# Performance work log

Hardware: AMD Instinct MI355X
Metric: run time of the kernel (lower is better)

## Reference

```python
import jax, jax.numpy as jnp
import numpy as np

S, H, E, DFF = 8192, 1024, 8, 4096
CAPACITY = (S * 1) // E  # capacity_factor=1.0, k=1 -> 1024 (>= min_capacity 4)


def setup_inputs() -> dict:
    key = jax.random.key(0)
    ks = jax.random.split(key, 6)
    sc_in = 1.0 / np.sqrt(H)
    sc_ff = 1.0 / np.sqrt(DFF)
    return {
        "hidden_states": jax.random.normal(ks[0], (S, H), dtype=jnp.float32),
        "wg": jax.random.normal(ks[1], (H, E), dtype=jnp.float32) * sc_in,
        "w1": jax.random.normal(ks[2], (E, H, DFF), dtype=jnp.float32) * sc_in,
        "b1": jnp.zeros((E, DFF), dtype=jnp.float32),
        "w2": jax.random.normal(ks[3], (E, DFF, H), dtype=jnp.float32) * sc_ff,
        "b2": jnp.zeros((E, H), dtype=jnp.float32),
    }


def _top1_gate(x, wg):
    # DeepSpeed top1gating (noisy_gate_policy=None, used_token=None)
    logits = x @ wg                                   # [S, E]
    gates = jax.nn.softmax(logits, axis=-1)           # [S, E]
    idx = jnp.argmax(gates, axis=-1)                  # [S]
    mask1 = jax.nn.one_hot(idx, E, dtype=gates.dtype) # [S, E]
    # load-balancing aux loss (uses pre-capacity mask)
    me = jnp.mean(gates, axis=0)
    ce = jnp.mean(mask1, axis=0)
    l_aux = jnp.sum(me * ce) * E
    # capacity-based token dropping
    locations1 = jnp.cumsum(mask1, axis=0) - 1.0      # position within expert
    mask1 = mask1 * (locations1 < CAPACITY)
    exp_counts = jnp.sum(mask1, axis=0).astype(jnp.int32)
    loc_s = jnp.sum(locations1 * mask1, axis=1).astype(jnp.int32)   # [S]
    loc_sc = jax.nn.one_hot(loc_s, CAPACITY, dtype=gates.dtype)     # [S, C]
    combine = jnp.einsum("se,sc->sec", gates * mask1, loc_sc)       # [S, E, C]
    dispatch = (combine > 0).astype(gates.dtype)
    return l_aux, combine, dispatch, exp_counts


def reference(hidden_states, wg, w1, b1, w2, b2):
    l_aux, combine, dispatch, exp_counts = _top1_gate(hidden_states, wg)
    # dispatch tokens to expert slots: [E, C, H]
    disp = jnp.einsum("sec,sh->ech", dispatch, hidden_states)
    # grouped expert FFN (GELU MLP)
    h1 = jax.nn.gelu(jnp.einsum("ech,ehf->ecf", disp, w1) + b1[:, None, :])
    eo = jnp.einsum("ecf,efh->ech", h1, w2) + b2[:, None, :]
    # combine back to token order, weighted by gate values
    out = jnp.einsum("sec,ech->sh", combine, eo)      # [S, H]
    # dropout prob = 0.0 -> identity
    return out, l_aux, exp_counts
```

## Files before the change

kernel.cpp:

```cpp
#include <hip/hip_runtime.h>

#define S_TOK 8192
#define H_DIM 1024
#define NE    8
#define CAP   1024
#define DFF   4096

typedef unsigned short u16;
typedef __bf16 bf16_t;
typedef bf16_t bf16x8 __attribute__((ext_vector_type(8)));
typedef float  f32x4  __attribute__((ext_vector_type(4)));

__device__ __forceinline__ u16 f2bf(float f) {
  union { float f; unsigned u; } a; a.f = f;
  unsigned u = a.u;
  u += 0x7fffu + ((u >> 16) & 1u);
  return (u16)(u >> 16);
}

__device__ __forceinline__ float gelu_tanh(float x) {
  const float c = 0.7978845608028654f;
  float t = tanhf(c * (x + 0.044715f * x * x * x));
  return 0.5f * x * (1.0f + t);
}

__global__ void gate_kernel(const float* __restrict__ x, const float* __restrict__ wg,
                            float* __restrict__ gate, int* __restrict__ expert,
                            int* __restrict__ rank, int* __restrict__ blockCnt,
                            float* __restrict__ blockMe) {
  __shared__ float sg[16][8];
  __shared__ int   se[16];
  int tid = threadIdx.x, lane = tid & 63, w = tid >> 6;
  int b = blockIdx.x;
  for (int j = 0; j < 4; ++j) {
    int t = w * 4 + j;
    int s = b * 16 + t;
    const float* xr = x + (size_t)s * H_DIM;
    float acc[8];
#pragma unroll
    for (int e = 0; e < 8; ++e) acc[e] = 0.f;
#pragma unroll
    for (int i = 0; i < 16; ++i) {
      int h = i * 64 + lane;
      float xv = xr[h];
      float4 wa = *(const float4*)(wg + h * 8);
      float4 wb = *(const float4*)(wg + h * 8 + 4);
      acc[0] += xv * wa.x; acc[1] += xv * wa.y; acc[2] += xv * wa.z; acc[3] += xv * wa.w;
      acc[4] += xv * wb.x; acc[5] += xv * wb.y; acc[6] += xv * wb.z; acc[7] += xv * wb.w;
    }
#pragma unroll
    for (int off = 32; off >= 1; off >>= 1)
#pragma unroll
      for (int e = 0; e < 8; ++e) acc[e] += __shfl_down(acc[e], off);
    if (lane == 0) {
      float mx = acc[0];
#pragma unroll
      for (int e = 1; e < 8; ++e) mx = fmaxf(mx, acc[e]);
      float g[8], Z = 0.f;
#pragma unroll
      for (int e = 0; e < 8; ++e) { g[e] = expf(acc[e] - mx); Z += g[e]; }
      int am = 0; float best = acc[0];
#pragma unroll
      for (int e = 1; e < 8; ++e) if (acc[e] > best) { best = acc[e]; am = e; }
      float inv = 1.f / Z;
#pragma unroll
      for (int e = 0; e < 8; ++e) sg[t][e] = g[e] * inv;
      se[t] = am;
      gate[s] = g[am] * inv;
      expert[s] = am;
    }
  }
  __syncthreads();
  if (tid < 16) {
    int e = se[tid], r = 0;
    for (int t2 = 0; t2 < tid; ++t2) r += (se[t2] == e) ? 1 : 0;
    rank[b * 16 + tid] = r;
  }
  if (tid < 8) {
    int c = 0; float m = 0.f;
#pragma unroll
    for (int t = 0; t < 16; ++t) { c += (se[t] == tid) ? 1 : 0; m += sg[t][tid]; }
    blockCnt[b * 8 + tid] = c;
    blockMe[b * 8 + tid] = m;
  }
}

__global__ void scan_kernel(const int* __restrict__ blockCnt, const float* __restrict__ blockMe,
                            int* __restrict__ blockOff, int* __restrict__ counts,
                            float* __restrict__ tail) {
  int tid = threadIdx.x;
  int e = tid >> 6, lane = tid & 63;
  int run = 0; float msum = 0.f;
  for (int c = 0; c < 8; ++c) {
    int b = c * 64 + lane;
    int v = blockCnt[b * 8 + e];
    float mv = blockMe[b * 8 + e];
    int sc = v;
#pragma unroll
    for (int off = 1; off < 64; off <<= 1) {
      int u = __shfl_up(sc, off);
      if (lane >= off) sc += u;
    }
    blockOff[b * 8 + e] = run + sc - v;
    run += __shfl(sc, 63);
#pragma unroll
    for (int off = 32; off >= 1; off >>= 1) mv += __shfl_down(mv, off);
    msum += __shfl(mv, 0);
  }
  __shared__ float sm[8];
  __shared__ int scnt[8];
  if (lane == 0) {
    sm[e] = msum; scnt[e] = run;
    counts[e] = run < CAP ? run : CAP;
  }
  __syncthreads();
  if (tid == 0) {
    float la = 0.f;
    for (int i = 0; i < 8; ++i)
      la += (sm[i] / (float)S_TOK) * ((float)scnt[i] / (float)S_TOK);
    tail[0] = la * (float)NE;
    for (int i = 0; i < 8; ++i) {
      int cc = scnt[i] < CAP ? scnt[i] : CAP;
      tail[1 + i] = (float)cc;
    }
  }
}

__global__ void assign_kernel(const int* __restrict__ expert, const int* __restrict__ rank,
                              const int* __restrict__ blockOff, int* __restrict__ slot_token) {
  int s = blockIdx.x * 256 + threadIdx.x;
  int e = expert[s];
  int pos = blockOff[(s >> 4) * 8 + e] + rank[s];
  if (pos < CAP) slot_token[e * CAP + pos] = s;
}

__global__ void gather_kernel(const float* __restrict__ x, const int* __restrict__ slot_token,
                              const int* __restrict__ counts, u16* __restrict__ disp) {
  int slot = blockIdx.x;
  int e = slot >> 10, c = slot & 1023;
  int t = threadIdx.x;
  ushort4 v4;
  if (c < counts[e]) {
    int s = slot_token[slot];
    float4 v = *(const float4*)(x + (size_t)s * H_DIM + t * 4);
    v4.x = f2bf(v.x); v4.y = f2bf(v.y); v4.z = f2bf(v.z); v4.w = f2bf(v.w);
  } else {
    v4.x = 0; v4.y = 0; v4.z = 0; v4.w = 0;
  }
  *(ushort4*)(disp + (size_t)slot * H_DIM + t * 4) = v4;
}

__global__ void transpose_convert(const float* __restrict__ src0, u16* __restrict__ dst0,
                                  int R, int C) {
  __shared__ float tile[64][65];
  int e = blockIdx.z;
  const float* src = src0 + (size_t)e * R * C;
  u16* dst = dst0 + (size_t)e * R * C;
  int c0 = blockIdx.x * 64, r0 = blockIdx.y * 64;
  int g = threadIdx.x & 15, rr = threadIdx.x >> 4;
#pragma unroll
  for (int p = 0; p < 4; ++p) {
    int r = rr + p * 16;
    float4 v = *(const float4*)(src + (size_t)(r0 + r) * C + c0 + g * 4);
    tile[r][g * 4 + 0] = v.x;
    tile[r][g * 4 + 1] = v.y;
    tile[r][g * 4 + 2] = v.z;
    tile[r][g * 4 + 3] = v.w;
  }
  __syncthreads();
#pragma unroll
  for (int p = 0; p < 4; ++p) {
    int c = rr + p * 16;
    ushort4 o;
    o.x = f2bf(tile[g * 4 + 0][c]);
    o.y = f2bf(tile[g * 4 + 1][c]);
    o.z = f2bf(tile[g * 4 + 2][c]);
    o.w = f2bf(tile[g * 4 + 3][c]);
    *(ushort4*)(dst + (size_t)(c0 + c) * R + r0 + g * 4) = o;
  }
}

__device__ __forceinline__ void stage_tile(const u16* g, int ldk, u16* lds) {
  int tid = threadIdx.x;
  int lane = tid & 63, w = tid >> 6;
#pragma unroll
  for (int r = 0; r < 2; ++r) {
    int p = (w * 2 + r) * 64 + lane;
    int row = p >> 2;
    int kq = (p & 3) ^ ((row >> 1) & 3);
    const u16* gp = g + (size_t)row * ldk + kq * 8;
    u16* lp = lds + (w * 2 + r) * 512;
    __builtin_amdgcn_global_load_lds((__attribute__((address_space(1))) int*)(gp),
                                     (__attribute__((address_space(3))) int*)(lp),
                                     16, 0, 0);
  }
}

template <int KDIM>
__device__ __forceinline__ void gemm_core(const u16* A, const u16* Bt, int lda, int ldb,
                                          u16* As, u16* Bs, f32x4 acc[4][4]) {
  int tid = threadIdx.x;
  int lane = tid & 63;
  int w = tid >> 6, wm = w >> 1, wn = w & 1;
  int q = lane >> 4, l15 = lane & 15;
  int aoff[4], boff[4];
#pragma unroll
  for (int t = 0; t < 4; ++t) {
    int ra = wm * 64 + t * 16 + l15;
    aoff[t] = ra * 32 + ((q ^ ((ra >> 1) & 3)) * 8);
    int rb = wn * 64 + t * 16 + l15;
    boff[t] = rb * 32 + ((q ^ ((rb >> 1) & 3)) * 8);
  }
  for (int kt = 0; kt < KDIM; kt += 32) {
    stage_tile(A + kt, lda, As);
    stage_tile(Bt + kt, ldb, Bs);
    __syncthreads();
    bf16x8 af[4], bfr[4];
#pragma unroll
    for (int t = 0; t < 4; ++t) af[t] = *(const bf16x8*)(As + aoff[t]);
#pragma unroll
    for (int t = 0; t < 4; ++t) bfr[t] = *(const bf16x8*)(Bs + boff[t]);
#pragma unroll
    for (int mt = 0; mt < 4; ++mt)
#pragma unroll
      for (int nt = 0; nt < 4; ++nt)
        acc[mt][nt] = __builtin_amdgcn_mfma_f32_16x16x32_bf16(af[mt], bfr[nt], acc[mt][nt], 0, 0, 0);
    __syncthreads();
  }
}

__global__ __launch_bounds__(256, 2) void gemm1_kernel(const u16* __restrict__ disp,
                                                       const u16* __restrict__ w1t,
                                                       const float* __restrict__ b1,
                                                       u16* __restrict__ h1) {
  __shared__ __align__(16) u16 As[4096];
  __shared__ __align__(16) u16 Bs[4096];
  int e = blockIdx.z;
  int m0 = blockIdx.y * 128, n0 = blockIdx.x * 128;
  const u16* A  = disp + (size_t)e * CAP * H_DIM + (size_t)m0 * H_DIM;
  const u16* Bt = w1t + (size_t)e * DFF * H_DIM + (size_t)n0 * H_DIM;
  f32x4 acc[4][4];
  f32x4 zero = {0.f, 0.f, 0.f, 0.f};
#pragma unroll
  for (int i = 0; i < 4; ++i)
#pragma unroll
    for (int j = 0; j < 4; ++j) acc[i][j] = zero;
  gemm_core<H_DIM>(A, Bt, H_DIM, H_DIM, As, Bs, acc);
  int tid = threadIdx.x, lane = tid & 63, w = tid >> 6, wm = w >> 1, wn = w & 1;
  int q = lane >> 4, l15 = lane & 15;
  const float* b1e = b1 + e * DFF;
  u16* out = h1 + (size_t)e * CAP * DFF;
#pragma unroll
  for (int mt = 0; mt < 4; ++mt)
#pragma unroll
    for (int nt = 0; nt < 4; ++nt) {
      int col = n0 + wn * 64 + nt * 16 + l15;
      float bias = b1e[col];
#pragma unroll
      for (int r = 0; r < 4; ++r) {
        int row = m0 + wm * 64 + mt * 16 + q * 4 + r;
        out[(size_t)row * DFF + col] = f2bf(gelu_tanh(acc[mt][nt][r] + bias));
      }
    }
}

__global__ __launch_bounds__(512, 4) void gemm2_kernel(const u16* __restrict__ h1,
                                                       const u16* __restrict__ w2t,
                                                       const float* __restrict__ b2,
                                                       const int* __restrict__ slot_token,
                                                       const float* __restrict__ gate,
                                                       const int* __restrict__ counts,
                                                       float* __restrict__ out) {
  __shared__ __align__(16) u16 As[4096];
  __shared__ __align__(16) u16 Bs[4096];
  int e = blockIdx.z;
  int m0 = blockIdx.y * 128, n0 = blockIdx.x * 128;
  const u16* A  = h1 + (size_t)e * CAP * DFF + (size_t)m0 * DFF;
  const u16* Bt = w2t + (size_t)e * H_DIM * DFF + (size_t)n0 * DFF;
  int tid = threadIdx.x, lane = tid & 63, w = tid >> 6;
  int wm = w >> 2, wn = w & 3;
  int q = lane >> 4, l15 = lane & 15;
  f32x4 acc[4][2];
  f32x4 zero = {0.f, 0.f, 0.f, 0.f};
#pragma unroll
  for (int i = 0; i < 4; ++i) { acc[i][0] = zero; acc[i][1] = zero; }

  const u16* gsrc = (w < 4) ? A : Bt;
  u16* ldst = (w < 4) ? As : Bs;
  int q4 = w & 3;
  const u16* gp0[2]; u16* lp[2];
#pragma unroll
  for (int r = 0; r < 2; ++r) {
    int p = (q4 * 2 + r) * 64 + lane;
    int srow = p >> 2;
    int skq = (p & 3) ^ ((srow >> 1) & 3);
    gp0[r] = gsrc + (size_t)srow * DFF + skq * 8;
    lp[r] = ldst + (q4 * 2 + r) * 512;
  }

  int aoff[4], boff[2];
#pragma unroll
  for (int t = 0; t < 4; ++t) {
    int ra = wm * 64 + t * 16 + l15;
    aoff[t] = ra * 32 + ((q ^ ((ra >> 1) & 3)) * 8);
  }
#pragma unroll
  for (int t = 0; t < 2; ++t) {
    int rb = wn * 32 + t * 16 + l15;
    boff[t] = rb * 32 + ((q ^ ((rb >> 1) & 3)) * 8);
  }

  for (int kt = 0; kt < DFF; kt += 32) {
#pragma unroll
    for (int r = 0; r < 2; ++r)
      __builtin_amdgcn_global_load_lds((__attribute__((address_space(1))) int*)(gp0[r] + kt),
                                       (__attribute__((address_space(3))) int*)(lp[r]),
                                       16, 0, 0);
    __syncthreads();
    bf16x8 af[4], bfr[2];
#pragma unroll
    for (int t = 0; t < 4; ++t) af[t] = *(const bf16x8*)(As + aoff[t]);
#pragma unroll
    for (int t = 0; t < 2; ++t) bfr[t] = *(const bf16x8*)(Bs + boff[t]);
#pragma unroll
    for (int mt = 0; mt < 4; ++mt)
#pragma unroll
      for (int nt = 0; nt < 2; ++nt)
        acc[mt][nt] = __builtin_amdgcn_mfma_f32_16x16x32_bf16(af[mt], bfr[nt], acc[mt][nt], 0, 0, 0);
    __syncthreads();
  }

  int cnt = counts[e];
  const float* b2e = b2 + e * H_DIM;
#pragma unroll
  for (int mt = 0; mt < 4; ++mt) {
    int tok[4]; float gv[4];
#pragma unroll
    for (int r = 0; r < 4; ++r) {
      int c = m0 + wm * 64 + mt * 16 + q * 4 + r;
      if (c < cnt) { int s = slot_token[e * CAP + c]; tok[r] = s; gv[r] = gate[s]; }
      else { tok[r] = -1; gv[r] = 0.f; }
    }
#pragma unroll
    for (int nt = 0; nt < 2; ++nt) {
      int col = n0 + wn * 32 + nt * 16 + l15;
      float bias = b2e[col];
#pragma unroll
      for (int r = 0; r < 4; ++r)
        if (tok[r] >= 0)
          out[(size_t)tok[r] * H_DIM + col] = gv[r] * (acc[mt][nt][r] + bias);
    }
  }
}

extern "C" void kernel_launch(void* const* d_in, const int* in_sizes, int n_in,
                              void* d_out, int out_size, void* d_ws, size_t ws_size,
                              hipStream_t stream) {
  const float* x  = (const float*)d_in[0];
  const float* wg = (const float*)d_in[1];
  const float* w1 = (const float*)d_in[2];
  const float* b1 = (const float*)d_in[3];
  const float* w2 = (const float*)d_in[4];
  const float* b2 = (const float*)d_in[5];
  float* out = (float*)d_out;
  char* ws = (char*)d_ws;
  const size_t MB = 1024 * 1024;
  u16* w1t  = (u16*)(ws);
  u16* w2t  = (u16*)(ws + 64 * MB);
  u16* disp = (u16*)(ws + 128 * MB);
  u16* h1   = (u16*)(ws + 144 * MB);
  char* sm = ws + 208 * MB;
  float* gate      = (float*)(sm);
  int*   expert    = (int*)(sm + 32 * 1024);
  int*   rank      = (int*)(sm + 64 * 1024);
  int*   slot_tok  = (int*)(sm + 96 * 1024);
  int*   blockCnt  = (int*)(sm + 128 * 1024);
  int*   blockOff  = (int*)(sm + 144 * 1024);
  float* blockMe   = (float*)(sm + 160 * 1024);
  int*   counts    = (int*)(sm + 176 * 1024);

  hipMemsetAsync(d_out, 0, (size_t)out_size * sizeof(float), stream);
  gate_kernel<<<512, 256, 0, stream>>>(x, wg, gate, expert, rank, blockCnt, blockMe);
  scan_kernel<<<1, 512, 0, stream>>>(blockCnt, blockMe, blockOff, counts,
                                     out + (size_t)S_TOK * H_DIM);
  assign_kernel<<<32, 256, 0, stream>>>(expert, rank, blockOff, slot_tok);
  gather_kernel<<<8192, 256, 0, stream>>>(x, slot_tok, counts, disp);
  transpose_convert<<<dim3(DFF / 64, H_DIM / 64, NE), 256, 0, stream>>>(w1, w1t, H_DIM, DFF);
  transpose_convert<<<dim3(H_DIM / 64, DFF / 64, NE), 256, 0, stream>>>(w2, w2t, DFF, H_DIM);
  gemm1_kernel<<<dim3(DFF / 128, CAP / 128, NE), 256, 0, stream>>>(disp, w1t, b1, h1);
  gemm2_kernel<<<dim3(H_DIM / 128, CAP / 128, NE), 512, 0, stream>>>(h1, w2t, b2,
                                                                     slot_tok, gate, counts, out);
}
```

Before: 620.8 us.

## Double-buffer LDS with K=64 tiles and swizzle block order in expert GEMMs

Both expert GEMM kernels now use double-buffered LDS tiles with a K step of 64, so the next tile's global_load_lds is issued before the current tile's MFMAs. This halves the barrier count and overlaps memory with compute. The launch grid is flattened and remapped so that consecutive blocks land on different experts and tiles, spreading L2/HBM traffic, and the LDS XOR swizzle is widened to 8 slots. LDS use per block grows to 64KB, which may reduce occupancy against the stated launch bounds.

```diff
diff --git a/kernel.cpp b/kernel.cpp
--- a/kernel.cpp
+++ b/kernel.cpp
@@ -180,74 +180,93 @@
   }
 }
 
-__device__ __forceinline__ void stage_tile(const u16* g, int ldk, u16* lds) {
-  int tid = threadIdx.x;
-  int lane = tid & 63, w = tid >> 6;
-#pragma unroll
-  for (int r = 0; r < 2; ++r) {
-    int p = (w * 2 + r) * 64 + lane;
-    int row = p >> 2;
-    int kq = (p & 3) ^ ((row >> 1) & 3);
-    const u16* gp = g + (size_t)row * ldk + kq * 8;
-    u16* lp = lds + (w * 2 + r) * 512;
-    __builtin_amdgcn_global_load_lds((__attribute__((address_space(1))) int*)(gp),
-                                     (__attribute__((address_space(3))) int*)(lp),
-                                     16, 0, 0);
-  }
-}
-
-template <int KDIM>
-__device__ __forceinline__ void gemm_core(const u16* A, const u16* Bt, int lda, int ldb,
-                                          u16* As, u16* Bs, f32x4 acc[4][4]) {
-  int tid = threadIdx.x;
-  int lane = tid & 63;
-  int w = tid >> 6, wm = w >> 1, wn = w & 1;
-  int q = lane >> 4, l15 = lane & 15;
-  int aoff[4], boff[4];
-#pragma unroll
-  for (int t = 0; t < 4; ++t) {
-    int ra = wm * 64 + t * 16 + l15;
-    aoff[t] = ra * 32 + ((q ^ ((ra >> 1) & 3)) * 8);
-    int rb = wn * 64 + t * 16 + l15;
-    boff[t] = rb * 32 + ((q ^ ((rb >> 1) & 3)) * 8);
-  }
-  for (int kt = 0; kt < KDIM; kt += 32) {
-    stage_tile(A + kt, lda, As);
-    stage_tile(Bt + kt, ldb, Bs);
-    __syncthreads();
-    bf16x8 af[4], bfr[4];
-#pragma unroll
-    for (int t = 0; t < 4; ++t) af[t] = *(const bf16x8*)(As + aoff[t]);
-#pragma unroll
-    for (int t = 0; t < 4; ++t) bfr[t] = *(const bf16x8*)(Bs + boff[t]);
-#pragma unroll
-    for (int mt = 0; mt < 4; ++mt)
-#pragma unroll
-      for (int nt = 0; nt < 4; ++nt)
-        acc[mt][nt] = __builtin_amdgcn_mfma_f32_16x16x32_bf16(af[mt], bfr[nt], acc[mt][nt], 0, 0, 0);
-    __syncthreads();
-  }
-}
-
 __global__ __launch_bounds__(256, 2) void gemm1_kernel(const u16* __restrict__ disp,
                                                        const u16* __restrict__ w1t,
                                                        const float* __restrict__ b1,
                                                        u16* __restrict__ h1) {
-  __shared__ __align__(16) u16 As[4096];
-  __shared__ __align__(16) u16 Bs[4096];
-  int e = blockIdx.z;
-  int m0 = blockIdx.y * 128, n0 = blockIdx.x * 128;
+  __shared__ __align__(16) u16 As[2][8192];
+  __shared__ __align__(16) u16 Bs[2][8192];
+  int flat = blockIdx.x;
+  int swz = (flat & 7) * 256 + (flat >> 3);
+  int e  = swz >> 8;
+  int r  = swz & 255;
+  int bx = r >> 3;
+  int by = r & 7;
+  int m0 = by * 128, n0 = bx * 128;
   const u16* A  = disp + (size_t)e * CAP * H_DIM + (size_t)m0 * H_DIM;
   const u16* Bt = w1t + (size_t)e * DFF * H_DIM + (size_t)n0 * H_DIM;
+
+  int tid = threadIdx.x, lane = tid & 63, w = tid >> 6;
+  int wm = w >> 1, wn = w & 1, q = lane >> 4, l15 = lane & 15;
+
+  const u16* gpA[4]; const u16* gpB[4]; int lofs[4];
+#pragma unroll
+  for (int i = 0; i < 4; ++i) {
+    int p = (w * 4 + i) * 64 + lane;
+    int row = p >> 3, slot = p & 7;
+    int kq = slot ^ (row & 7);
+    gpA[i] = A + (size_t)row * H_DIM + kq * 8;
+    gpB[i] = Bt + (size_t)row * H_DIM + kq * 8;
+    lofs[i] = (w * 4 + i) * 512;
+  }
+
+  int aoff[2][4], boff[2][4];
+#pragma unroll
+  for (int t = 0; t < 4; ++t) {
+    int ra = wm * 64 + t * 16 + l15;
+    int rb = wn * 64 + t * 16 + l15;
+#pragma unroll
+    for (int s = 0; s < 2; ++s) {
+      aoff[s][t] = ra * 64 + (((s * 4) + q) ^ (ra & 7)) * 8;
+      boff[s][t] = rb * 64 + (((s * 4) + q) ^ (rb & 7)) * 8;
+    }
+  }
+
   f32x4 acc[4][4];
   f32x4 zero = {0.f, 0.f, 0.f, 0.f};
 #pragma unroll
   for (int i = 0; i < 4; ++i)
 #pragma unroll
     for (int j = 0; j < 4; ++j) acc[i][j] = zero;
-  gemm_core<H_DIM>(A, Bt, H_DIM, H_DIM, As, Bs, acc);
-  int tid = threadIdx.x, lane = tid & 63, w = tid >> 6, wm = w >> 1, wn = w & 1;
-  int q = lane >> 4, l15 = lane & 15;
+
+#pragma unroll
+  for (int i = 0; i < 4; ++i) {
+    __builtin_amdgcn_global_load_lds((__attribute__((address_space(1))) int*)(gpA[i]),
+                                     (__attribute__((address_space(3))) int*)(&As[0][0] + lofs[i]), 16, 0, 0);
+    __builtin_amdgcn_global_load_lds((__attribute__((address_space(1))) int*)(gpB[i]),
+                                     (__attribute__((address_space(3))) int*)(&Bs[0][0] + lofs[i]), 16, 0, 0);
+  }
+  __syncthreads();
+
+  int cur = 0;
+  for (int kt = 0; kt < H_DIM; kt += 64) {
+    if (kt + 64 < H_DIM) {
+      int nxt = cur ^ 1;
+#pragma unroll
+      for (int i = 0; i < 4; ++i) {
+        __builtin_amdgcn_global_load_lds((__attribute__((address_space(1))) int*)(gpA[i] + kt + 64),
+                                         (__attribute__((address_space(3))) int*)(&As[nxt][0] + lofs[i]), 16, 0, 0);
+        __builtin_amdgcn_global_load_lds((__attribute__((address_space(1))) int*)(gpB[i] + kt + 64),
+                                         (__attribute__((address_space(3))) int*)(&Bs[nxt][0] + lofs[i]), 16, 0, 0);
+      }
+    }
+#pragma unroll
+    for (int s = 0; s < 2; ++s) {
+      bf16x8 af[4], bfr[4];
+#pragma unroll
+      for (int t = 0; t < 4; ++t) af[t] = *(const bf16x8*)(&As[cur][0] + aoff[s][t]);
+#pragma unroll
+      for (int t = 0; t < 4; ++t) bfr[t] = *(const bf16x8*)(&Bs[cur][0] + boff[s][t]);
+#pragma unroll
+      for (int mt = 0; mt < 4; ++mt)
+#pragma unroll
+        for (int nt = 0; nt < 4; ++nt)
+          acc[mt][nt] = __builtin_amdgcn_mfma_f32_16x16x32_bf16(af[mt], bfr[nt], acc[mt][nt], 0, 0, 0);
+    }
+    __syncthreads();
+    cur ^= 1;
+  }
+
   const float* b1e = b1 + e * DFF;
   u16* out = h1 + (size_t)e * CAP * DFF;
 #pragma unroll
@@ -257,9 +276,9 @@
       int col = n0 + wn * 64 + nt * 16 + l15;
       float bias = b1e[col];
 #pragma unroll
-      for (int r = 0; r < 4; ++r) {
-        int row = m0 + wm * 64 + mt * 16 + q * 4 + r;
-        out[(size_t)row * DFF + col] = f2bf(gelu_tanh(acc[mt][nt][r] + bias));
+      for (int rr = 0; rr < 4; ++rr) {
+        int row = m0 + wm * 64 + mt * 16 + q * 4 + rr;
+        out[(size_t)row * DFF + col] = f2bf(gelu_tanh(acc[mt][nt][rr] + bias));
       }
     }
 }
@@ -271,10 +290,15 @@
                                                        const float* __restrict__ gate,
                                                        const int* __restrict__ counts,
                                                        float* __restrict__ out) {
-  __shared__ __align__(16) u16 As[4096];
-  __shared__ __align__(16) u16 Bs[4096];
-  int e = blockIdx.z;
-  int m0 = blockIdx.y * 128, n0 = blockIdx.x * 128;
+  __shared__ __align__(16) u16 As[2][8192];
+  __shared__ __align__(16) u16 Bs[2][8192];
+  int flat = blockIdx.x;
+  int swz = (flat & 7) * 64 + (flat >> 3);
+  int e  = swz >> 6;
+  int r  = swz & 63;
+  int bx = r & 7;
+  int by = r >> 3;
+  int m0 = by * 128, n0 = bx * 128;
   const u16* A  = h1 + (size_t)e * CAP * DFF + (size_t)m0 * DFF;
   const u16* Bt = w2t + (size_t)e * H_DIM * DFF + (size_t)n0 * DFF;
   int tid = threadIdx.x, lane = tid & 63, w = tid >> 6;
@@ -286,48 +310,68 @@
   for (int i = 0; i < 4; ++i) { acc[i][0] = zero; acc[i][1] = zero; }
 
   const u16* gsrc = (w < 4) ? A : Bt;
-  u16* ldst = (w < 4) ? As : Bs;
+  int isA = (w < 4) ? 1 : 0;
   int q4 = w & 3;
-  const u16* gp0[2]; u16* lp[2];
-#pragma unroll
-  for (int r = 0; r < 2; ++r) {
-    int p = (q4 * 2 + r) * 64 + lane;
-    int srow = p >> 2;
-    int skq = (p & 3) ^ ((srow >> 1) & 3);
-    gp0[r] = gsrc + (size_t)srow * DFF + skq * 8;
-    lp[r] = ldst + (q4 * 2 + r) * 512;
-  }
-
-  int aoff[4], boff[2];
+  const u16* gp[4]; int lofs[4];
+#pragma unroll
+  for (int i = 0; i < 4; ++i) {
+    int p = (q4 * 4 + i) * 64 + lane;
+    int row = p >> 3, slot = p & 7;
+    int kq = slot ^ (row & 7);
+    gp[i] = gsrc + (size_t)row * DFF + kq * 8;
+    lofs[i] = (q4 * 4 + i) * 512;
+  }
+
+  int aoff[2][4], boff[2][2];
 #pragma unroll
   for (int t = 0; t < 4; ++t) {
     int ra = wm * 64 + t * 16 + l15;
-    aoff[t] = ra * 32 + ((q ^ ((ra >> 1) & 3)) * 8);
+#pragma unroll
+    for (int s = 0; s < 2; ++s)
+      aoff[s][t] = ra * 64 + (((s * 4) + q) ^ (ra & 7)) * 8;
   }
 #pragma unroll
   for (int t = 0; t < 2; ++t) {
     int rb = wn * 32 + t * 16 + l15;
-    boff[t] = rb * 32 + ((q ^ ((rb >> 1) & 3)) * 8);
-  }
-
-  for (int kt = 0; kt < DFF; kt += 32) {
-#pragma unroll
-    for (int r = 0; r < 2; ++r)
-      __builtin_amdgcn_global_load_lds((__attribute__((address_space(1))) int*)(gp0[r] + kt),
-                                       (__attribute__((address_space(3))) int*)(lp[r]),
-                                       16, 0, 0);
+#pragma unroll
+    for (int s = 0; s < 2; ++s)
+      boff[s][t] = rb * 64 + (((s * 4) + q) ^ (rb & 7)) * 8;
+  }
+
+  {
+    u16* sb = isA ? &As[0][0] : &Bs[0][0];
+#pragma unroll
+    for (int i = 0; i < 4; ++i)
+      __builtin_amdgcn_global_load_lds((__attribute__((address_space(1))) int*)(gp[i]),
+                                       (__attribute__((address_space(3))) int*)(sb + lofs[i]), 16, 0, 0);
+  }
+  __syncthreads();
+
+  int cur = 0;
+  for (int kt = 0; kt < DFF; kt += 64) {
+    if (kt + 64 < DFF) {
+      int nxt = cur ^ 1;
+      u16* sb = isA ? &As[nxt][0] : &Bs[nxt][0];
+#pragma unroll
+      for (int i = 0; i < 4; ++i)
+        __builtin_amdgcn_global_load_lds((__attribute__((address_space(1))) int*)(gp[i] + kt + 64),
+                                         (__attribute__((address_space(3))) int*)(sb + lofs[i]), 16, 0, 0);
+    }
+#pragma unroll
+    for (int s = 0; s < 2; ++s) {
+      bf16x8 af[4], bfr[2];
+#pragma unroll
+      for (int t = 0; t < 4; ++t) af[t] = *(const bf16x8*)(&As[cur][0] + aoff[s][t]);
+#pragma unroll
+      for (int t = 0; t < 2; ++t) bfr[t] = *(const bf16x8*)(&Bs[cur][0] + boff[s][t]);
+#pragma unroll
+      for (int mt = 0; mt < 4; ++mt)
+#pragma unroll
+        for (int nt = 0; nt < 2; ++nt)
+          acc[mt][nt] = __builtin_amdgcn_mfma_f32_16x16x32_bf16(af[mt], bfr[nt], acc[mt][nt], 0, 0, 0);
+    }
     __syncthreads();
-    bf16x8 af[4], bfr[2];
-#pragma unroll
-    for (int t = 0; t < 4; ++t) af[t] = *(const bf16x8*)(As + aoff[t]);
-#pragma unroll
-    for (int t = 0; t < 2; ++t) bfr[t] = *(const bf16x8*)(Bs + boff[t]);
-#pragma unroll
-    for (int mt = 0; mt < 4; ++mt)
-#pragma unroll
-      for (int nt = 0; nt < 2; ++nt)
-        acc[mt][nt] = __builtin_amdgcn_mfma_f32_16x16x32_bf16(af[mt], bfr[nt], acc[mt][nt], 0, 0, 0);
-    __syncthreads();
+    cur ^= 1;
   }
 
   int cnt = counts[e];
@@ -336,19 +380,19 @@
   for (int mt = 0; mt < 4; ++mt) {
     int tok[4]; float gv[4];
 #pragma unroll
-    for (int r = 0; r < 4; ++r) {
-      int c = m0 + wm * 64 + mt * 16 + q * 4 + r;
-      if (c < cnt) { int s = slot_token[e * CAP + c]; tok[r] = s; gv[r] = gate[s]; }
-      else { tok[r] = -1; gv[r] = 0.f; }
+    for (int rr = 0; rr < 4; ++rr) {
+      int c = m0 + wm * 64 + mt * 16 + q * 4 + rr;
+      if (c < cnt) { int s = slot_token[e * CAP + c]; tok[rr] = s; gv[rr] = gate[s]; }
+      else { tok[rr] = -1; gv[rr] = 0.f; }
     }
 #pragma unroll
     for (int nt = 0; nt < 2; ++nt) {
       int col = n0 + wn * 32 + nt * 16 + l15;
       float bias = b2e[col];
 #pragma unroll
-      for (int r = 0; r < 4; ++r)
-        if (tok[r] >= 0)
-          out[(size_t)tok[r] * H_DIM + col] = gv[r] * (acc[mt][nt][r] + bias);
+      for (int rr = 0; rr < 4; ++rr)
+        if (tok[rr] >= 0)
+          out[(size_t)tok[rr] * H_DIM + col] = gv[rr] * (acc[mt][nt][rr] + bias);
     }
   }
 }
@@ -387,7 +431,6 @@
   gather_kernel<<<8192, 256, 0, stream>>>(x, slot_tok, counts, disp);
   transpose_convert<<<dim3(DFF / 64, H_DIM / 64, NE), 256, 0, stream>>>(w1, w1t, H_DIM, DFF);
   transpose_convert<<<dim3(H_DIM / 64, DFF / 64, NE), 256, 0, stream>>>(w2, w2t, DFF, H_DIM);
-  gemm1_kernel<<<dim3(DFF / 128, CAP / 128, NE), 256, 0, stream>>>(disp, w1t, b1, h1);
-  gemm2_kernel<<<dim3(H_DIM / 128, CAP / 128, NE), 512, 0, stream>>>(h1, w2t, b2,
-                                                                     slot_tok, gate, counts, out);
-}
+  gemm1_kernel<<<2048, 256, 0, stream>>>(disp, w1t, b1, h1);
+  gemm2_kernel<<<512, 512, 0, stream>>>(h1, w2t, b2, slot_tok, gate, counts, out);
+}
```

Measured after the change: 610.6 us. About the same (-1.6%).
